# Performance work log

Hardware: AMD Instinct MI355X
Metric: run time of the kernel (lower is better)

The kernel has to match this reference:

```python
import jax, jax.numpy as jnp
import numpy as np

HEADS = 4
HID = 64
IN_DIM = 128
N_WIRES, N_TERM, N_ACT = 50, 20, 10
NEG_SLOPE = 0.2


def gat_conv(x, src, dst, ea, W, We, a_src, a_dst, a_edge, bias, concat):
    """PyG GATConv with edge features, add_self_loops=True, fill_value='mean'."""
    N = x.shape[0]
    H, F = a_src.shape
    # --- add self loops; self-loop edge_attr = mean of incoming edge_attr ---
    deg = jax.ops.segment_sum(jnp.ones((ea.shape[0],), x.dtype), dst, num_segments=N)
    loop_attr = jax.ops.segment_sum(ea, dst, num_segments=N) / jnp.maximum(deg, 1.0)[:, None]
    ar = jnp.arange(N)
    src = jnp.concatenate([src, ar])
    dst = jnp.concatenate([dst, ar])
    ea = jnp.concatenate([ea, loop_attr], axis=0)
    # --- linear transforms ---
    h = (x @ W).reshape(N, H, F)                      # [N,H,F]
    a_s = jnp.einsum('nhf,hf->nh', h, a_src)          # [N,H]
    a_d = jnp.einsum('nhf,hf->nh', h, a_dst)
    he = (ea @ We).reshape(-1, H, F)                  # [E2,H,F]
    a_e = jnp.einsum('ehf,hf->eh', he, a_edge)        # [E2,H]
    # --- attention logits + softmax over edges grouped by destination ---
    alpha = jax.nn.leaky_relu(a_s[src] + a_d[dst] + a_e, negative_slope=NEG_SLOPE)
    amax = jax.ops.segment_max(alpha, dst, num_segments=N)
    ex = jnp.exp(alpha - amax[dst])
    denom = jax.ops.segment_sum(ex, dst, num_segments=N)
    alpha = ex / (denom[dst] + 1e-16)                 # [E2,H]
    # --- message passing: gather src feats, weight, scatter-sum to dst ---
    out = jax.ops.segment_sum(h[src] * alpha[..., None], dst, num_segments=N)  # [N,H,F]
    out = out.reshape(N, H * F) if concat else out.mean(axis=1)
    return out + bias


def setup_inputs() -> dict:
    key = jax.random.key(0)
    ks = jax.random.split(key, 24)
    N, E = 20000, 320000
    x = jax.random.normal(ks[0], (N, IN_DIM), jnp.float32)
    edge_index = jax.random.randint(ks[1], (2, E), 0, N, dtype=jnp.int64)
    edge_attr = jax.random.normal(ks[2], (E, 2), jnp.float32)
    s = 0.1
    p = {
        'W1': jax.random.normal(ks[3], (IN_DIM, HEADS * HID)) * s,
        'We1': jax.random.normal(ks[4], (2, HEADS * HID)) * s,
        'as1': jax.random.normal(ks[5], (HEADS, HID)) * s,
        'ad1': jax.random.normal(ks[6], (HEADS, HID)) * s,
        'ae1': jax.random.normal(ks[7], (HEADS, HID)) * s,
        'b1': jnp.zeros((HEADS * HID,), jnp.float32),
        'W2': jax.random.normal(ks[8], (HEADS * HID, HEADS * HID)) * s,
        'We2': jax.random.normal(ks[9], (2, HEADS * HID)) * s,
        'as2': jax.random.normal(ks[10], (HEADS, HID)) * s,
        'ad2': jax.random.normal(ks[11], (HEADS, HID)) * s,
        'ae2': jax.random.normal(ks[12], (HEADS, HID)) * s,
        'b2': jnp.zeros((HID,), jnp.float32),
        'Ww': jax.random.normal(ks[13], (HID, N_WIRES)) * s,
        'bw': jnp.zeros((N_WIRES,), jnp.float32),
        'Wt': jax.random.normal(ks[14], (HID, N_TERM)) * s,
        'bt': jnp.zeros((N_TERM,), jnp.float32),
        'Wa': jax.random.normal(ks[15], (HID, N_ACT)) * s,
        'ba': jnp.zeros((N_ACT,), jnp.float32),
    }
    return {'x': x, 'edge_index': edge_index, 'edge_attr': edge_attr, **p}


def reference(x, edge_index, edge_attr, W1, We1, as1, ad1, ae1, b1,
              W2, We2, as2, ad2, ae2, b2, Ww, bw, Wt, bt, Wa, ba):
    src, dst = edge_index[0], edge_index[1]
    h = jax.nn.elu(gat_conv(x, src, dst, edge_attr, W1, We1, as1, ad1, ae1, b1, True))
    h = jax.nn.elu(gat_conv(h, src, dst, edge_attr, W2, We2, as2, ad2, ae2, b2, False))
    wire_logits = h @ Ww + bw
    terminal_logits = h @ Wt + bt
    action_logits = h @ Wa + ba
    return (wire_logits, terminal_logits, action_logits)
```

## Files before the change

### kernel.cpp

```cpp
#include <hip/hip_runtime.h>
#include <math.h>

#define N_NODES 20000
#define N_EDGES 320000
#define D1      256
#define SCAP    64
#define NSCAT   1250
#define NPREP   (NSCAT + 385 + 32)

typedef __attribute__((ext_vector_type(8))) short    bf16x8;
typedef __attribute__((ext_vector_type(4))) float    f32x4;
typedef __attribute__((ext_vector_type(8))) unsigned short u16x8;

__device__ inline float wred_sum(float v) {
#pragma unroll
  for (int o = 32; o > 0; o >>= 1) v += __shfl_xor(v, o, 64);
  return v;
}

__device__ inline unsigned short f2b(float v) {
  unsigned u = __float_as_uint(v);
  unsigned r = (u + 0x7fffu + ((u >> 16) & 1u)) >> 16;
  return (unsigned short)r;
}
__device__ inline float b2f(unsigned short h) {
  return __uint_as_float(((unsigned)h) << 16);
}

__global__ __launch_bounds__(256) void k_prep(
    const int* __restrict__ ei, const float* __restrict__ ea,
    int* __restrict__ deg, int4* __restrict__ slot,
    const float* __restrict__ W1, unsigned short* __restrict__ WT1h,
    unsigned short* __restrict__ WT1l,
    const float* __restrict__ W2, unsigned short* __restrict__ WT2h,
    unsigned short* __restrict__ WT2l,
    const float* __restrict__ We1, const float* __restrict__ ae1,
    const float* __restrict__ We2, const float* __restrict__ ae2,
    float* __restrict__ qb,
    const float* __restrict__ Ww, const float* __restrict__ Wt,
    const float* __restrict__ Wa,
    const float* __restrict__ bw, const float* __restrict__ bt,
    const float* __restrict__ ba,
    unsigned short* __restrict__ WallTh, unsigned short* __restrict__ WallTl,
    float* __restrict__ biasAll) {
  int bid = blockIdx.x, t = threadIdx.x;
  if (bid < NSCAT) {
    int e = bid * 256 + t;
    int s = ei[e], d = ei[N_EDGES + e];
    float2 e2 = *(const float2*)&ea[e * 2];
    int pos = atomicAdd(&deg[d], 1);
    if (pos < SCAP) {
      int4 rec;
      rec.x = s; rec.y = __float_as_int(e2.x);
      rec.z = __float_as_int(e2.y); rec.w = 0;
      slot[(size_t)d * SCAP + pos] = rec;
    }
  } else if (bid < NSCAT + 128) {
    int i = (bid - NSCAT) * 256 + t;
    int k = i >> 8, n = i & 255;
    float v = W1[i];
    unsigned short h = f2b(v);
    WT1h[n * 128 + k] = h;
    WT1l[n * 128 + k] = f2b(v - b2f(h));
  } else if (bid < NSCAT + 384) {
    int i = (bid - NSCAT - 128) * 256 + t;
    int k = i >> 8, n = i & 255;
    float v = W2[i];
    unsigned short h = f2b(v);
    WT2h[n * 256 + k] = h;
    WT2l[n * 256 + k] = f2b(v - b2f(h));
  } else if (bid == NSCAT + 384) {
    int lane = t & 63, w = t >> 6;
    const float* We = (w >> 1) ? We2 : We1;
    const float* ae = (w >> 1) ? ae2 : ae1;
    int c = w & 1;
#pragma unroll
    for (int h = 0; h < 4; h++) {
      float p = We[c * D1 + h * 64 + lane] * ae[h * 64 + lane];
      p = wred_sum(p);
      if (lane == 0) qb[(w >> 1) * 8 + c * 4 + h] = p;
    }
    if (t < 80) biasAll[t] = (t < 50) ? bw[t] : (t < 70) ? bt[t - 50] : ba[t - 70];
  } else {
    int i = (bid - NSCAT - 385) * 256 + t;
    int j = i >> 6, f = i & 63;
    float v = 0.f;
    if (j < 50)      v = Ww[f * 50 + j];
    else if (j < 70) v = Wt[f * 20 + (j - 50)];
    else if (j < 80) v = Wa[f * 10 + (j - 70)];
    unsigned short h = f2b(v);
    WallTh[j * 64 + f] = h;
    WallTl[j * 64 + f] = f2b(v - b2f(h));
  }
}

#define LDK 40
template <bool AF32>
__global__ __launch_bounds__(256) void k_gemm_mfma(
    const float* __restrict__ Af, const unsigned short* __restrict__ Ah,
    const unsigned short* __restrict__ BTh, const unsigned short* __restrict__ BTl,
    unsigned short* __restrict__ Chi,
    const float* __restrict__ asw, const float* __restrict__ adw,
    float* __restrict__ asb, float* __restrict__ adb,
    int M, int K) {
  __shared__ unsigned short sAh[128 * LDK];
  __shared__ unsigned short sBh[128 * LDK], sBl[128 * LDK];
  int tid = threadIdx.x;
  int lane = tid & 63, wid = tid >> 6;
  int wr = wid >> 1, wc = wid & 1;
  int row0 = blockIdx.y * 128, col0 = blockIdx.x * 128;
  int aRow = wr * 64, bRow = wc * 64;

  f32x4 acc[4][4];
#pragma unroll
  for (int i = 0; i < 4; i++)
#pragma unroll
    for (int j = 0; j < 4; j++) acc[i][j] = (f32x4){0.f, 0.f, 0.f, 0.f};

  int c0i = tid * 2;
  int r0 = c0i >> 2, ko0 = (c0i & 3) * 8;
  int c1i = tid * 2 + 1;
  int r1 = c1i >> 2, ko1 = (c1i & 3) * 8;
  int q8 = (lane >> 4) * 8;
  int rsel = lane & 15;

  const u16x8 z8 = {0, 0, 0, 0, 0, 0, 0, 0};
  int ga0 = row0 + r0, ga1 = row0 + r1;
  bool va0 = ga0 < M, va1 = ga1 < M;
  size_t arow0 = (size_t)ga0 * K, arow1 = (size_t)ga1 * K;
  size_t brow0 = (size_t)(col0 + r0) * K, brow1 = (size_t)(col0 + r1) * K;

  auto ldA = [&](size_t rowoff, bool valid, int kk) -> u16x8 {
    if (!valid) return z8;
    if constexpr (AF32) {
      float4 f0 = *(const float4*)&Af[rowoff + kk];
      float4 f1 = *(const float4*)&Af[rowoff + kk + 4];
      u16x8 r;
      r[0] = f2b(f0.x); r[1] = f2b(f0.y); r[2] = f2b(f0.z); r[3] = f2b(f0.w);
      r[4] = f2b(f1.x); r[5] = f2b(f1.y); r[6] = f2b(f1.z); r[7] = f2b(f1.w);
      return r;
    } else {
      return *(const u16x8*)&Ah[rowoff + kk];
    }
  };

  u16x8 ca0 = ldA(arow0, va0, ko0), ca1 = ldA(arow1, va1, ko1);
  u16x8 cbh0 = *(const u16x8*)&BTh[brow0 + ko0];
  u16x8 cbl0 = *(const u16x8*)&BTl[brow0 + ko0];
  u16x8 cbh1 = *(const u16x8*)&BTh[brow1 + ko1];
  u16x8 cbl1 = *(const u16x8*)&BTl[brow1 + ko1];

  for (int k0 = 0; k0 < K; k0 += 32) {
    *(u16x8*)&sAh[r0 * LDK + ko0] = ca0;
    *(u16x8*)&sAh[r1 * LDK + ko1] = ca1;
    *(u16x8*)&sBh[r0 * LDK + ko0] = cbh0;
    *(u16x8*)&sBl[r0 * LDK + ko0] = cbl0;
    *(u16x8*)&sBh[r1 * LDK + ko1] = cbh1;
    *(u16x8*)&sBl[r1 * LDK + ko1] = cbl1;
    __syncthreads();

    if (k0 + 32 < K) {
      int kn = k0 + 32;
      ca0 = ldA(arow0, va0, kn + ko0);
      ca1 = ldA(arow1, va1, kn + ko1);
      cbh0 = *(const u16x8*)&BTh[brow0 + kn + ko0];
      cbl0 = *(const u16x8*)&BTl[brow0 + kn + ko0];
      cbh1 = *(const u16x8*)&BTh[brow1 + kn + ko1];
      cbl1 = *(const u16x8*)&BTl[brow1 + kn + ko1];
    }

    bf16x8 fah[4], fbh[4], fbl[4];
#pragma unroll
    for (int i = 0; i < 4; i++) {
      int ar = aRow + i * 16 + rsel;
      int br = bRow + i * 16 + rsel;
      fah[i] = *(const bf16x8*)&sAh[ar * LDK + q8];
      fbh[i] = *(const bf16x8*)&sBh[br * LDK + q8];
      fbl[i] = *(const bf16x8*)&sBl[br * LDK + q8];
    }
#pragma unroll
    for (int i = 0; i < 4; i++)
#pragma unroll
      for (int j = 0; j < 4; j++) {
        acc[i][j] = __builtin_amdgcn_mfma_f32_16x16x32_bf16(fah[i], fbh[j], acc[i][j], 0, 0, 0);
        acc[i][j] = __builtin_amdgcn_mfma_f32_16x16x32_bf16(fah[i], fbl[j], acc[i][j], 0, 0, 0);
      }
    __syncthreads();
  }

  int rq = (lane >> 4) * 4;
  int head = (col0 + bRow) >> 6;
  float sa[4], sd[4];
#pragma unroll
  for (int j = 0; j < 4; j++) {
    sa[j] = asw[head * 64 + j * 16 + rsel];
    sd[j] = adw[head * 64 + j * 16 + rsel];
  }
#pragma unroll
  for (int i = 0; i < 4; i++) {
#pragma unroll
    for (int j = 0; j < 4; j++) {
      int gcol = col0 + bRow + j * 16 + rsel;
#pragma unroll
      for (int r = 0; r < 4; r++) {
        int grow = row0 + aRow + i * 16 + rq + r;
        if (grow < M) Chi[(size_t)grow * D1 + gcol] = f2b(acc[i][j][r]);
      }
    }
#pragma unroll
    for (int r = 0; r < 4; r++) {
      float ps = 0.f, pd = 0.f;
#pragma unroll
      for (int j = 0; j < 4; j++) {
        ps = fmaf(acc[i][j][r], sa[j], ps);
        pd = fmaf(acc[i][j][r], sd[j], pd);
      }
#pragma unroll
      for (int o = 1; o < 16; o <<= 1) {
        ps += __shfl_xor(ps, o, 64);
        pd += __shfl_xor(pd, o, 64);
      }
      int grow = row0 + aRow + i * 16 + rq + r;
      if ((lane & 15) == 0 && grow < M) {
        asb[grow * 4 + head] = ps;
        adb[grow * 4 + head] = pd;
      }
    }
  }
}

__global__ __launch_bounds__(256) void k_heads_mfma(
    const unsigned short* __restrict__ Ah, const unsigned short* __restrict__ Al,
    const unsigned short* __restrict__ BTh, const unsigned short* __restrict__ BTl,
    const float* __restrict__ biasAll, float* __restrict__ out, int M) {
  __shared__ unsigned short sAh[128 * LDK], sAl[128 * LDK];
  __shared__ unsigned short sBh[128 * LDK], sBl[128 * LDK];
  const int K = 64;
  int tid = threadIdx.x;
  int lane = tid & 63, wid = tid >> 6;
  int wr = wid >> 1, wc = wid & 1;
  int row0 = blockIdx.x * 128;
  int aRow = wr * 64, bRow = wc * 64;

  f32x4 acc[4][4];
#pragma unroll
  for (int i = 0; i < 4; i++)
#pragma unroll
    for (int j = 0; j < 4; j++) acc[i][j] = (f32x4){0.f, 0.f, 0.f, 0.f};

  int c0i = tid * 2;
  int r0 = c0i >> 2, ko0 = (c0i & 3) * 8;
  int c1i = tid * 2 + 1;
  int r1 = c1i >> 2, ko1 = (c1i & 3) * 8;
  int q8 = (lane >> 4) * 8;
  int rsel = lane & 15;

  for (int k0 = 0; k0 < K; k0 += 32) {
    u16x8 z = {0, 0, 0, 0, 0, 0, 0, 0};
    int ga0 = row0 + r0, ga1 = row0 + r1;
    u16x8 vah0 = (ga0 < M) ? *(const u16x8*)&Ah[(size_t)ga0 * K + k0 + ko0] : z;
    u16x8 val0 = (ga0 < M) ? *(const u16x8*)&Al[(size_t)ga0 * K + k0 + ko0] : z;
    u16x8 vah1 = (ga1 < M) ? *(const u16x8*)&Ah[(size_t)ga1 * K + k0 + ko1] : z;
    u16x8 val1 = (ga1 < M) ? *(const u16x8*)&Al[(size_t)ga1 * K + k0 + ko1] : z;
    u16x8 vbh0 = *(const u16x8*)&BTh[(size_t)r0 * K + k0 + ko0];
    u16x8 vbl0 = *(const u16x8*)&BTl[(size_t)r0 * K + k0 + ko0];
    u16x8 vbh1 = *(const u16x8*)&BTh[(size_t)r1 * K + k0 + ko1];
    u16x8 vbl1 = *(const u16x8*)&BTl[(size_t)r1 * K + k0 + ko1];
    *(u16x8*)&sAh[r0 * LDK + ko0] = vah0;
    *(u16x8*)&sAl[r0 * LDK + ko0] = val0;
    *(u16x8*)&sAh[r1 * LDK + ko1] = vah1;
    *(u16x8*)&sAl[r1 * LDK + ko1] = val1;
    *(u16x8*)&sBh[r0 * LDK + ko0] = vbh0;
    *(u16x8*)&sBl[r0 * LDK + ko0] = vbl0;
    *(u16x8*)&sBh[r1 * LDK + ko1] = vbh1;
    *(u16x8*)&sBl[r1 * LDK + ko1] = vbl1;
    __syncthreads();

    bf16x8 fah[4], fal[4], fbh[4], fbl[4];
#pragma unroll
    for (int i = 0; i < 4; i++) {
      int ar = aRow + i * 16 + rsel;
      int br = bRow + i * 16 + rsel;
      fah[i] = *(const bf16x8*)&sAh[ar * LDK + q8];
      fal[i] = *(const bf16x8*)&sAl[ar * LDK + q8];
      fbh[i] = *(const bf16x8*)&sBh[br * LDK + q8];
      fbl[i] = *(const bf16x8*)&sBl[br * LDK + q8];
    }
#pragma unroll
    for (int i = 0; i < 4; i++)
#pragma unroll
      for (int j = 0; j < 4; j++) {
        acc[i][j] = __builtin_amdgcn_mfma_f32_16x16x32_bf16(fah[i], fbh[j], acc[i][j], 0, 0, 0);
        acc[i][j] = __builtin_amdgcn_mfma_f32_16x16x32_bf16(fah[i], fbl[j], acc[i][j], 0, 0, 0);
        acc[i][j] = __builtin_amdgcn_mfma_f32_16x16x32_bf16(fal[i], fbh[j], acc[i][j], 0, 0, 0);
      }
    __syncthreads();
  }

  int rq = (lane >> 4) * 4;
#pragma unroll
  for (int j = 0; j < 4; j++) {
    int gcol = bRow + j * 16 + rsel;
    if (gcol < 80) {
      float bj = biasAll[gcol];
      float* op; int cols, jj;
      if (gcol < 50)      { op = out;                 cols = 50; jj = gcol; }
      else if (gcol < 70) { op = out + N_NODES * 50;  cols = 20; jj = gcol - 50; }
      else                { op = out + N_NODES * 70;  cols = 10; jj = gcol - 70; }
#pragma unroll
      for (int i = 0; i < 4; i++) {
#pragma unroll
        for (int r = 0; r < 4; r++) {
          int grow = row0 + aRow + i * 16 + rq + r;
          if (grow < M) op[(size_t)grow * cols + jj] = acc[i][j][r] + bj;
        }
      }
    }
  }
}

template <bool CONCAT>
__global__ __launch_bounds__(256) void k_aggregate(
    const unsigned short* __restrict__ feath,
    const int* __restrict__ deg_arr, const int4* __restrict__ slot,
    const float* __restrict__ asb, const float* __restrict__ adb,
    const float* __restrict__ q, const float* __restrict__ bias,
    unsigned short* __restrict__ outh,
    unsigned short* __restrict__ outf_h, unsigned short* __restrict__ outf_l) {
  __shared__ float slog[4][SCAP][4];
  __shared__ int   ssrc[4][SCAP];
  int t = threadIdx.x, lane = t & 63, w = t >> 6;
  int n = blockIdx.x * 4 + w;
  int deg = min(deg_arr[n], SCAP);

  float4 qv0 = *(const float4*)q;
  float4 qv1 = *(const float4*)(q + 4);
  float4 ad4 = *(const float4*)&adb[(size_t)n * 4];
  float4 asn = *(const float4*)&asb[(size_t)n * 4];

  int degR = (deg + 15) & ~15;
  if (degR == 0) degR = 16;
  int   sreg = n;
  float e0v = 0.f, e1v = 0.f;
  if (lane < degR) {
    if (lane < deg) {
      int4 rec = slot[(size_t)n * SCAP + lane];
      sreg = rec.x; e0v = __int_as_float(rec.y); e1v = __int_as_float(rec.z);
    }
    ssrc[w][lane] = sreg;
  }
  float l0 = -1e30f, l1 = -1e30f, l2 = -1e30f, l3 = -1e30f;
  if (lane < deg) {
    float4 as4 = *(const float4*)&asb[(size_t)sreg * 4];
    l0 = as4.x + ad4.x + e0v * qv0.x + e1v * qv1.x; l0 = (l0 > 0.f) ? l0 : 0.2f * l0;
    l1 = as4.y + ad4.y + e0v * qv0.y + e1v * qv1.y; l1 = (l1 > 0.f) ? l1 : 0.2f * l1;
    l2 = as4.z + ad4.z + e0v * qv0.z + e1v * qv1.z; l2 = (l2 > 0.f) ? l2 : 0.2f * l2;
    l3 = as4.w + ad4.w + e0v * qv0.w + e1v * qv1.w; l3 = (l3 > 0.f) ? l3 : 0.2f * l3;
  }
  float dinv = 1.f / fmaxf((float)deg, 1.f);
  float e0m = wred_sum(e0v) * dinv;
  float e1m = wred_sum(e1v) * dinv;
  float ls[4];
  ls[0] = asn.x + ad4.x + e0m * qv0.x + e1m * qv1.x;
  ls[1] = asn.y + ad4.y + e0m * qv0.y + e1m * qv1.y;
  ls[2] = asn.z + ad4.z + e0m * qv0.z + e1m * qv1.z;
  ls[3] = asn.w + ad4.w + e0m * qv0.w + e1m * qv1.w;
#pragma unroll
  for (int h = 0; h < 4; h++) ls[h] = (ls[h] > 0.f) ? ls[h] : 0.2f * ls[h];
  float ex[4] = {__expf(l0), __expf(l1), __expf(l2), __expf(l3)};
  float inv[4], wself[4];
#pragma unroll
  for (int h = 0; h < 4; h++) {
    float eself = __expf(ls[h]);
    float ss = wred_sum(ex[h]) + eself;
    inv[h] = 1.f / (ss + 1e-16f);
    wself[h] = eself * inv[h];
  }
  if (lane < degR) {
    *(f32x4*)&slog[w][lane][0] = (f32x4){ex[0] * inv[0], ex[1] * inv[1],
                                         ex[2] * inv[2], ex[3] * inv[3]};
  }
  int es = lane >> 5, cg = lane & 31, hh = cg >> 3;
  const unsigned short* fb = feath + cg * 8;
  float acc8[8] = {};
  for (int j0 = 0; j0 < degR; j0 += 16) {
    u16x8 f[8];
#pragma unroll
    for (int q8 = 0; q8 < 8; q8++)
      f[q8] = *(const u16x8*)&fb[(size_t)ssrc[w][j0 + 2 * q8 + es] * D1];
#pragma unroll
    for (int q8 = 0; q8 < 8; q8++) {
      float ww = slog[w][j0 + 2 * q8 + es][hh];
#pragma unroll
      for (int k = 0; k < 8; k++) acc8[k] = fmaf(ww, b2f((unsigned short)f[q8][k]), acc8[k]);
    }
  }
  if (es == 0) {
    u16x8 fs = *(const u16x8*)&fb[(size_t)n * D1];
    float ws2 = wself[hh];
#pragma unroll
    for (int k = 0; k < 8; k++) acc8[k] = fmaf(ws2, b2f((unsigned short)fs[k]), acc8[k]);
  }
#pragma unroll
  for (int k = 0; k < 8; k++) acc8[k] += __shfl_xor(acc8[k], 32, 64);
  if constexpr (CONCAT) {
    if (es == 0) {
      u16x8 hi8;
#pragma unroll
      for (int k = 0; k < 8; k++) {
        float v2 = acc8[k] + bias[cg * 8 + k];
        v2 = (v2 > 0.f) ? v2 : (__expf(v2) - 1.f);
        hi8[k] = f2b(v2);
      }
      *(u16x8*)&outh[(size_t)n * D1 + cg * 8] = hi8;
    }
  } else {
#pragma unroll
    for (int k = 0; k < 8; k++) {
      acc8[k] += __shfl_xor(acc8[k], 8, 64);
      acc8[k] += __shfl_xor(acc8[k], 16, 64);
    }
    if (es == 0 && cg < 8) {
      u16x8 hi8, lo8;
#pragma unroll
      for (int k = 0; k < 8; k++) {
        float v2 = acc8[k] * 0.25f + bias[cg * 8 + k];
        v2 = (v2 > 0.f) ? v2 : (__expf(v2) - 1.f);
        unsigned short hh2 = f2b(v2);
        hi8[k] = hh2;
        lo8[k] = f2b(v2 - b2f(hh2));
      }
      *(u16x8*)&outf_h[(size_t)n * 64 + cg * 8] = hi8;
      *(u16x8*)&outf_l[(size_t)n * 64 + cg * 8] = lo8;
    }
  }
}

extern "C" void kernel_launch(void* const* d_in, const int* in_sizes, int n_in,
                              void* d_out, int out_size, void* d_ws, size_t ws_size,
                              hipStream_t stream) {
  const float* x   = (const float*)d_in[0];
  const int*   ei  = (const int*)d_in[1];
  const float* ea  = (const float*)d_in[2];
  const float* W1  = (const float*)d_in[3];
  const float* We1 = (const float*)d_in[4];
  const float* as1 = (const float*)d_in[5];
  const float* ad1 = (const float*)d_in[6];
  const float* ae1 = (const float*)d_in[7];
  const float* b1  = (const float*)d_in[8];
  const float* W2  = (const float*)d_in[9];
  const float* We2 = (const float*)d_in[10];
  const float* as2 = (const float*)d_in[11];
  const float* ad2 = (const float*)d_in[12];
  const float* ae2 = (const float*)d_in[13];
  const float* b2  = (const float*)d_in[14];
  const float* Ww  = (const float*)d_in[15];
  const float* bw  = (const float*)d_in[16];
  const float* Wt  = (const float*)d_in[17];
  const float* bt  = (const float*)d_in[18];
  const float* Wa  = (const float*)d_in[19];
  const float* ba  = (const float*)d_in[20];
  float* out = (float*)d_out;

  char* ws = (char*)d_ws;
  size_t off = 0;
  auto alloc = [&](size_t bytes) {
    void* p = ws + off;
    off += (bytes + 255) & ~(size_t)255;
    return p;
  };
  unsigned short* Ah     = (unsigned short*)alloc((size_t)N_NODES * D1 * 2);
  unsigned short* Bfh    = (unsigned short*)alloc((size_t)N_NODES * D1 * 2);
  unsigned short* h2h    = (unsigned short*)alloc((size_t)N_NODES * 64 * 2);
  unsigned short* h2l    = (unsigned short*)alloc((size_t)N_NODES * 64 * 2);
  unsigned short* WT1h   = (unsigned short*)alloc((size_t)128 * 256 * 2);
  unsigned short* WT1l   = (unsigned short*)alloc((size_t)128 * 256 * 2);
  unsigned short* WT2h   = (unsigned short*)alloc((size_t)256 * 256 * 2);
  unsigned short* WT2l   = (unsigned short*)alloc((size_t)256 * 256 * 2);
  unsigned short* WallTh = (unsigned short*)alloc((size_t)128 * 64 * 2);
  unsigned short* WallTl = (unsigned short*)alloc((size_t)128 * 64 * 2);
  float*          biasAll= (float*)alloc(80 * 4);
  int4*  slot    = (int4*)alloc((size_t)N_NODES * SCAP * 16);
  int*   deg     = (int*)alloc((size_t)N_NODES * 4);
  float* asb     = (float*)alloc((size_t)N_NODES * 4 * 4);
  float* adb     = (float*)alloc((size_t)N_NODES * 4 * 4);
  float* qb      = (float*)alloc(64);

  hipMemsetAsync(deg, 0, (size_t)N_NODES * 4, stream);

  k_prep<<<NPREP, 256, 0, stream>>>(
      ei, ea, deg, slot,
      W1, WT1h, WT1l, W2, WT2h, WT2l, We1, ae1, We2, ae2, qb,
      Ww, Wt, Wa, bw, bt, ba, WallTh, WallTl, biasAll);

  dim3 ggemm(2, (N_NODES + 127) / 128);

  k_gemm_mfma<true><<<ggemm, 256, 0, stream>>>(x, nullptr, WT1h, WT1l, Ah,
                                               as1, ad1, asb, adb, N_NODES, 128);
  k_aggregate<true><<<N_NODES / 4, 256, 0, stream>>>(
      Ah, deg, slot, asb, adb, qb, b1, Bfh, nullptr, nullptr);

  k_gemm_mfma<false><<<ggemm, 256, 0, stream>>>(nullptr, Bfh, WT2h, WT2l, Ah,
                                                as2, ad2, asb, adb, N_NODES, 256);
  k_aggregate<false><<<N_NODES / 4, 256, 0, stream>>>(
      Ah, deg, slot, asb, adb, qb + 8, b2, nullptr, h2h, h2l);

  k_heads_mfma<<<(N_NODES + 127) / 128, 256, 0, stream>>>(
      h2h, h2l, WallTh, WallTl, biasAll, out, N_NODES);
}
```

Before: 224.6 us.

## Merge edge scatter into first GEMM launch and fold deg memset into prep

The edge-bucketing scatter moves out of k_prep into a new k_fused1 kernel. Its blocks run alongside the layer-1 MFMA GEMM blocks in one launch, so the atomic scatter can overlap with matrix work. The hipMemsetAsync of deg is replaced by extra zeroing blocks in k_prep, which removes one launch. The cost is a more complex heterogeneous kernel whose GEMM blocks carry the scatter's register and LDS footprint, which may affect occupancy and scheduling.

```diff
diff --git a/kernel.cpp b/kernel.cpp
--- a/kernel.cpp
+++ b/kernel.cpp
@@ -5,8 +5,9 @@
 #define N_EDGES 320000
 #define D1      256
 #define SCAP    64
+#define NGEMM1  314
 #define NSCAT   1250
-#define NPREP   (NSCAT + 385 + 32)
+#define NPREP   496
 
 typedef __attribute__((ext_vector_type(8))) short    bf16x8;
 typedef __attribute__((ext_vector_type(4))) float    f32x4;
@@ -28,8 +29,7 @@
 }
 
 __global__ __launch_bounds__(256) void k_prep(
-    const int* __restrict__ ei, const float* __restrict__ ea,
-    int* __restrict__ deg, int4* __restrict__ slot,
+    int* __restrict__ deg,
     const float* __restrict__ W1, unsigned short* __restrict__ WT1h,
     unsigned short* __restrict__ WT1l,
     const float* __restrict__ W2, unsigned short* __restrict__ WT2h,
@@ -44,8 +44,65 @@
     unsigned short* __restrict__ WallTh, unsigned short* __restrict__ WallTl,
     float* __restrict__ biasAll) {
   int bid = blockIdx.x, t = threadIdx.x;
-  if (bid < NSCAT) {
-    int e = bid * 256 + t;
+  if (bid < 128) {
+    int i = bid * 256 + t;
+    int k = i >> 8, n = i & 255;
+    float v = W1[i];
+    unsigned short h = f2b(v);
+    WT1h[n * 128 + k] = h;
+    WT1l[n * 128 + k] = f2b(v - b2f(h));
+  } else if (bid < 384) {
+    int i = (bid - 128) * 256 + t;
+    int k = i >> 8, n = i & 255;
+    float v = W2[i];
+    unsigned short h = f2b(v);
+    WT2h[n * 256 + k] = h;
+    WT2l[n * 256 + k] = f2b(v - b2f(h));
+  } else if (bid == 384) {
+    int lane = t & 63, w = t >> 6;
+    const float* We = (w >> 1) ? We2 : We1;
+    const float* ae = (w >> 1) ? ae2 : ae1;
+    int c = w & 1;
+#pragma unroll
+    for (int h = 0; h < 4; h++) {
+      float p = We[c * D1 + h * 64 + lane] * ae[h * 64 + lane];
+      p = wred_sum(p);
+      if (lane == 0) qb[(w >> 1) * 8 + c * 4 + h] = p;
+    }
+    if (t < 80) biasAll[t] = (t < 50) ? bw[t] : (t < 70) ? bt[t - 50] : ba[t - 70];
+  } else if (bid < 417) {
+    int i = (bid - 385) * 256 + t;
+    int j = i >> 6, f = i & 63;
+    float v = 0.f;
+    if (j < 50)      v = Ww[f * 50 + j];
+    else if (j < 70) v = Wt[f * 20 + (j - 50)];
+    else if (j < 80) v = Wa[f * 10 + (j - 70)];
+    unsigned short h = f2b(v);
+    WallTh[j * 64 + f] = h;
+    WallTl[j * 64 + f] = f2b(v - b2f(h));
+  } else {
+    int i = (bid - 417) * 256 + t;
+    if (i < N_NODES) deg[i] = 0;
+  }
+}
+
+#define LDK 40
+
+__global__ __launch_bounds__(256) void k_fused1(
+    const float* __restrict__ Af,
+    const unsigned short* __restrict__ BTh, const unsigned short* __restrict__ BTl,
+    unsigned short* __restrict__ Chi,
+    const float* __restrict__ asw, const float* __restrict__ adw,
+    float* __restrict__ asb, float* __restrict__ adb, int M,
+    const int* __restrict__ ei, const float* __restrict__ ea,
+    int* __restrict__ deg, int4* __restrict__ slot) {
+  __shared__ unsigned short sAh[128 * LDK];
+  __shared__ unsigned short sBh[128 * LDK], sBl[128 * LDK];
+  const int K = 128;
+  int bid = blockIdx.x, tid = threadIdx.x;
+
+  if (bid >= NGEMM1) {
+    int e = (bid - NGEMM1) * 256 + tid;
     int s = ei[e], d = ei[N_EDGES + e];
     float2 e2 = *(const float2*)&ea[e * 2];
     int pos = atomicAdd(&deg[d], 1);
@@ -55,49 +112,130 @@
       rec.z = __float_as_int(e2.y); rec.w = 0;
       slot[(size_t)d * SCAP + pos] = rec;
     }
-  } else if (bid < NSCAT + 128) {
-    int i = (bid - NSCAT) * 256 + t;
-    int k = i >> 8, n = i & 255;
-    float v = W1[i];
-    unsigned short h = f2b(v);
-    WT1h[n * 128 + k] = h;
-    WT1l[n * 128 + k] = f2b(v - b2f(h));
-  } else if (bid < NSCAT + 384) {
-    int i = (bid - NSCAT - 128) * 256 + t;
-    int k = i >> 8, n = i & 255;
-    float v = W2[i];
-    unsigned short h = f2b(v);
-    WT2h[n * 256 + k] = h;
-    WT2l[n * 256 + k] = f2b(v - b2f(h));
-  } else if (bid == NSCAT + 384) {
-    int lane = t & 63, w = t >> 6;
-    const float* We = (w >> 1) ? We2 : We1;
-    const float* ae = (w >> 1) ? ae2 : ae1;
-    int c = w & 1;
-#pragma unroll
-    for (int h = 0; h < 4; h++) {
-      float p = We[c * D1 + h * 64 + lane] * ae[h * 64 + lane];
-      p = wred_sum(p);
-      if (lane == 0) qb[(w >> 1) * 8 + c * 4 + h] = p;
-    }
-    if (t < 80) biasAll[t] = (t < 50) ? bw[t] : (t < 70) ? bt[t - 50] : ba[t - 70];
-  } else {
-    int i = (bid - NSCAT - 385) * 256 + t;
-    int j = i >> 6, f = i & 63;
-    float v = 0.f;
-    if (j < 50)      v = Ww[f * 50 + j];
-    else if (j < 70) v = Wt[f * 20 + (j - 50)];
-    else if (j < 80) v = Wa[f * 10 + (j - 70)];
-    unsigned short h = f2b(v);
-    WallTh[j * 64 + f] = h;
-    WallTl[j * 64 + f] = f2b(v - b2f(h));
-  }
-}
-
-#define LDK 40
-template <bool AF32>
+    return;
+  }
+
+  int lane = tid & 63, wid = tid >> 6;
+  int wr = wid >> 1, wc = wid & 1;
+  int row0 = (bid >> 1) * 128, col0 = (bid & 1) * 128;
+  int aRow = wr * 64, bRow = wc * 64;
+
+  f32x4 acc[4][4];
+#pragma unroll
+  for (int i = 0; i < 4; i++)
+#pragma unroll
+    for (int j = 0; j < 4; j++) acc[i][j] = (f32x4){0.f, 0.f, 0.f, 0.f};
+
+  int c0i = tid * 2;
+  int r0 = c0i >> 2, ko0 = (c0i & 3) * 8;
+  int c1i = tid * 2 + 1;
+  int r1 = c1i >> 2, ko1 = (c1i & 3) * 8;
+  int q8 = (lane >> 4) * 8;
+  int rsel = lane & 15;
+
+  const u16x8 z8 = {0, 0, 0, 0, 0, 0, 0, 0};
+  int ga0 = row0 + r0, ga1 = row0 + r1;
+  bool va0 = ga0 < M, va1 = ga1 < M;
+  size_t arow0 = (size_t)ga0 * K, arow1 = (size_t)ga1 * K;
+  size_t brow0 = (size_t)(col0 + r0) * K, brow1 = (size_t)(col0 + r1) * K;
+
+  auto ldA = [&](size_t rowoff, bool valid, int kk) -> u16x8 {
+    if (!valid) return z8;
+    float4 f0 = *(const float4*)&Af[rowoff + kk];
+    float4 f1 = *(const float4*)&Af[rowoff + kk + 4];
+    u16x8 r;
+    r[0] = f2b(f0.x); r[1] = f2b(f0.y); r[2] = f2b(f0.z); r[3] = f2b(f0.w);
+    r[4] = f2b(f1.x); r[5] = f2b(f1.y); r[6] = f2b(f1.z); r[7] = f2b(f1.w);
+    return r;
+  };
+
+  u16x8 ca0 = ldA(arow0, va0, ko0), ca1 = ldA(arow1, va1, ko1);
+  u16x8 cbh0 = *(const u16x8*)&BTh[brow0 + ko0];
+  u16x8 cbl0 = *(const u16x8*)&BTl[brow0 + ko0];
+  u16x8 cbh1 = *(const u16x8*)&BTh[brow1 + ko1];
+  u16x8 cbl1 = *(const u16x8*)&BTl[brow1 + ko1];
+
+  for (int k0 = 0; k0 < K; k0 += 32) {
+    *(u16x8*)&sAh[r0 * LDK + ko0] = ca0;
+    *(u16x8*)&sAh[r1 * LDK + ko1] = ca1;
+    *(u16x8*)&sBh[r0 * LDK + ko0] = cbh0;
+    *(u16x8*)&sBl[r0 * LDK + ko0] = cbl0;
+    *(u16x8*)&sBh[r1 * LDK + ko1] = cbh1;
+    *(u16x8*)&sBl[r1 * LDK + ko1] = cbl1;
+    __syncthreads();
+
+    if (k0 + 32 < K) {
+      int kn = k0 + 32;
+      ca0 = ldA(arow0, va0, kn + ko0);
+      ca1 = ldA(arow1, va1, kn + ko1);
+      cbh0 = *(const u16x8*)&BTh[brow0 + kn + ko0];
+      cbl0 = *(const u16x8*)&BTl[brow0 + kn + ko0];
+      cbh1 = *(const u16x8*)&BTh[brow1 + kn + ko1];
+      cbl1 = *(const u16x8*)&BTl[brow1 + kn + ko1];
+    }
+
+    bf16x8 fah[4], fbh[4], fbl[4];
+#pragma unroll
+    for (int i = 0; i < 4; i++) {
+      int ar = aRow + i * 16 + rsel;
+      int br = bRow + i * 16 + rsel;
+      fah[i] = *(const bf16x8*)&sAh[ar * LDK + q8];
+      fbh[i] = *(const bf16x8*)&sBh[br * LDK + q8];
+      fbl[i] = *(const bf16x8*)&sBl[br * LDK + q8];
+    }
+#pragma unroll
+    for (int i = 0; i < 4; i++)
+#pragma unroll
+      for (int j = 0; j < 4; j++) {
+        acc[i][j] = __builtin_amdgcn_mfma_f32_16x16x32_bf16(fah[i], fbh[j], acc[i][j], 0, 0, 0);
+        acc[i][j] = __builtin_amdgcn_mfma_f32_16x16x32_bf16(fah[i], fbl[j], acc[i][j], 0, 0, 0);
+      }
+    __syncthreads();
+  }
+
+  int rq = (lane >> 4) * 4;
+  int head = (col0 + bRow) >> 6;
+  float sa[4], sd[4];
+#pragma unroll
+  for (int j = 0; j < 4; j++) {
+    sa[j] = asw[head * 64 + j * 16 + rsel];
+    sd[j] = adw[head * 64 + j * 16 + rsel];
+  }
+#pragma unroll
+  for (int i = 0; i < 4; i++) {
+#pragma unroll
+    for (int j = 0; j < 4; j++) {
+      int gcol = col0 + bRow + j * 16 + rsel;
+#pragma unroll
+      for (int r = 0; r < 4; r++) {
+        int grow = row0 + aRow + i * 16 + rq + r;
+        if (grow < M) Chi[(size_t)grow * D1 + gcol] = f2b(acc[i][j][r]);
+      }
+    }
+#pragma unroll
+    for (int r = 0; r < 4; r++) {
+      float ps = 0.f, pd = 0.f;
+#pragma unroll
+      for (int j = 0; j < 4; j++) {
+        ps = fmaf(acc[i][j][r], sa[j], ps);
+        pd = fmaf(acc[i][j][r], sd[j], pd);
+      }
+#pragma unroll
+      for (int o = 1; o < 16; o <<= 1) {
+        ps += __shfl_xor(ps, o, 64);
+        pd += __shfl_xor(pd, o, 64);
+      }
+      int grow = row0 + aRow + i * 16 + rq + r;
+      if ((lane & 15) == 0 && grow < M) {
+        asb[grow * 4 + head] = ps;
+        adb[grow * 4 + head] = pd;
+      }
+    }
+  }
+}
+
 __global__ __launch_bounds__(256) void k_gemm_mfma(
-    const float* __restrict__ Af, const unsigned short* __restrict__ Ah,
+    const unsigned short* __restrict__ Ah,
     const unsigned short* __restrict__ BTh, const unsigned short* __restrict__ BTl,
     unsigned short* __restrict__ Chi,
     const float* __restrict__ asw, const float* __restrict__ adw,
@@ -130,21 +268,8 @@
   size_t arow0 = (size_t)ga0 * K, arow1 = (size_t)ga1 * K;
   size_t brow0 = (size_t)(col0 + r0) * K, brow1 = (size_t)(col0 + r1) * K;
 
-  auto ldA = [&](size_t rowoff, bool valid, int kk) -> u16x8 {
-    if (!valid) return z8;
-    if constexpr (AF32) {
-      float4 f0 = *(const float4*)&Af[rowoff + kk];
-      float4 f1 = *(const float4*)&Af[rowoff + kk + 4];
-      u16x8 r;
-      r[0] = f2b(f0.x); r[1] = f2b(f0.y); r[2] = f2b(f0.z); r[3] = f2b(f0.w);
-      r[4] = f2b(f1.x); r[5] = f2b(f1.y); r[6] = f2b(f1.z); r[7] = f2b(f1.w);
-      return r;
-    } else {
-      return *(const u16x8*)&Ah[rowoff + kk];
-    }
-  };
-
-  u16x8 ca0 = ldA(arow0, va0, ko0), ca1 = ldA(arow1, va1, ko1);
+  u16x8 ca0 = va0 ? *(const u16x8*)&Ah[arow0 + ko0] : z8;
+  u16x8 ca1 = va1 ? *(const u16x8*)&Ah[arow1 + ko1] : z8;
   u16x8 cbh0 = *(const u16x8*)&BTh[brow0 + ko0];
   u16x8 cbl0 = *(const u16x8*)&BTl[brow0 + ko0];
   u16x8 cbh1 = *(const u16x8*)&BTh[brow1 + ko1];
@@ -161,8 +286,8 @@
 
     if (k0 + 32 < K) {
       int kn = k0 + 32;
-      ca0 = ldA(arow0, va0, kn + ko0);
-      ca1 = ldA(arow1, va1, kn + ko1);
+      ca0 = va0 ? *(const u16x8*)&Ah[arow0 + kn + ko0] : z8;
+      ca1 = va1 ? *(const u16x8*)&Ah[arow1 + kn + ko1] : z8;
       cbh0 = *(const u16x8*)&BTh[brow0 + kn + ko0];
       cbl0 = *(const u16x8*)&BTl[brow0 + kn + ko0];
       cbh1 = *(const u16x8*)&BTh[brow1 + kn + ko1];
@@ -486,22 +611,19 @@
   float* adb     = (float*)alloc((size_t)N_NODES * 4 * 4);
   float* qb      = (float*)alloc(64);
 
-  hipMemsetAsync(deg, 0, (size_t)N_NODES * 4, stream);
-
   k_prep<<<NPREP, 256, 0, stream>>>(
-      ei, ea, deg, slot,
-      W1, WT1h, WT1l, W2, WT2h, WT2l, We1, ae1, We2, ae2, qb,
+      deg, W1, WT1h, WT1l, W2, WT2h, WT2l, We1, ae1, We2, ae2, qb,
       Ww, Wt, Wa, bw, bt, ba, WallTh, WallTl, biasAll);
 
-  dim3 ggemm(2, (N_NODES + 127) / 128);
-
-  k_gemm_mfma<true><<<ggemm, 256, 0, stream>>>(x, nullptr, WT1h, WT1l, Ah,
-                                               as1, ad1, asb, adb, N_NODES, 128);
+  k_fused1<<<NGEMM1 + NSCAT, 256, 0, stream>>>(
+      x, WT1h, WT1l, Ah, as1, ad1, asb, adb, N_NODES, ei, ea, deg, slot);
+
   k_aggregate<true><<<N_NODES / 4, 256, 0, stream>>>(
       Ah, deg, slot, asb, adb, qb, b1, Bfh, nullptr, nullptr);
 
-  k_gemm_mfma<false><<<ggemm, 256, 0, stream>>>(nullptr, Bfh, WT2h, WT2l, Ah,
-                                                as2, ad2, asb, adb, N_NODES, 256);
+  dim3 ggemm(2, (N_NODES + 127) / 128);
+  k_gemm_mfma<<<ggemm, 256, 0, stream>>>(Bfh, WT2h, WT2l, Ah,
+                                         as2, ad2, asb, adb, N_NODES, 256);
   k_aggregate<false><<<N_NODES / 4, 256, 0, stream>>>(
       Ah, deg, slot, asb, adb, qb + 8, b2, nullptr, h2h, h2l);
 
```

New measurement: 218.0 us. 3.0% less time.
